# Optimization experiments

Measured on AMD Instinct MI355X. Metric: run time of the kernel, lower is better.

Reference implementation:

```python
import jax, jax.numpy as jnp
import numpy as np

HEAD_SIZE = 64
INPUT_SIZE = 1024
B, T = 8, 2048


def setup_inputs() -> dict:
    key = jax.random.key(0)
    kx, kq, kk, kv = jax.random.split(key, 4)
    x = jax.random.normal(kx, (B, T, INPUT_SIZE), dtype=jnp.float32)
    s = 1.0 / np.sqrt(INPUT_SIZE)
    Wq = jax.random.uniform(kq, (INPUT_SIZE, HEAD_SIZE), minval=-s, maxval=s, dtype=jnp.float32)
    Wk = jax.random.uniform(kk, (INPUT_SIZE, HEAD_SIZE), minval=-s, maxval=s, dtype=jnp.float32)
    Wv = jax.random.uniform(kv, (INPUT_SIZE, HEAD_SIZE), minval=-s, maxval=s, dtype=jnp.float32)
    return {"x": x, "Wq": Wq, "Wk": Wk, "Wv": Wv}


def reference(x, Wq, Wk, Wv):
    # Faithful to the torch module: scores = K @ Q^T (note: keys times queries^T),
    # causal mask on upper triangle of that matrix, softmax over last axis,
    # dropout treated as identity (eval), then scores @ V.
    q = jnp.einsum('bti,ih->bth', x, Wq)  # [B,T,H]
    k = jnp.einsum('bti,ih->bth', x, Wk)
    v = jnp.einsum('bti,ih->bth', x, Wv)
    scale = HEAD_SIZE ** -0.5
    scores = jnp.einsum('bth,bsh->bts', k, q) * scale  # [B,T,T] = K Q^T
    Tlen = x.shape[1]
    causal = jnp.tril(jnp.ones((Tlen, Tlen), dtype=bool))
    scores = jnp.where(causal, scores, -jnp.inf)
    w = jax.nn.softmax(scores, axis=-1)
    out = jnp.einsum('bts,bsh->bth', w, v)  # [B,T,H]
    return out
```

## Files before the change

kernel.cpp:

```cpp
#include <hip/hip_runtime.h>

typedef __bf16 bf16_t;
typedef bf16_t bf16x8 __attribute__((ext_vector_type(8)));
typedef float f32x4 __attribute__((ext_vector_type(4)));

#define NB 8
#define TT 2048
#define DIN 1024
#define HH 64
#define MM (NB * TT)

__device__ __forceinline__ unsigned short f2bf(float f) {
    unsigned int u = __float_as_uint(f);
    u += 0x7fffu + ((u >> 16) & 1u);
    return (unsigned short)(u >> 16);
}

__device__ __forceinline__ void async16(void* l, const void* g) {
    __builtin_amdgcn_global_load_lds(
        (const __attribute__((address_space(1))) unsigned int*)g,
        (__attribute__((address_space(3))) unsigned int*)l, 16, 0, 0);
}

__device__ __forceinline__ int block_detect_f32(const unsigned int* __restrict__ xw,
                                                int tid, int* sflag) {
    if (tid < 64) {
        unsigned int u = xw[tid];
        unsigned int e = (u >> 7) & 0xFFu;
        unsigned long long m = __ballot(e >= 100u && e <= 150u);
        if (tid == 0) *sflag = (__popcll(m) < 48) ? 1 : 0;
    }
    __syncthreads();
    return *sflag;
}

__global__ __launch_bounds__(256) void transpose_w_kernel(
    const void* __restrict__ Wq, const void* __restrict__ Wk,
    const void* __restrict__ Wv, const unsigned int* __restrict__ xw,
    unsigned short* __restrict__ Wt) {
    __shared__ int sflag;
    __shared__ unsigned short ts[64][68];
    const int tid = threadIdx.x;
    const int isf32 = block_detect_f32(xw, tid, &sflag);
    const int w = blockIdx.x >> 4, kt = blockIdx.x & 15;
    const void* W = (w == 0) ? Wq : (w == 1) ? Wk : Wv;
    const int kk = tid >> 4, nn = (tid & 15) * 4;
#pragma unroll
    for (int j = 0; j < 4; ++j) {
        int k = kk + j * 16;
        if (isf32) {
            float4 f = *(const float4*)((const float*)W + (size_t)(kt * 64 + k) * 64 + nn);
            ts[k][nn + 0] = f2bf(f.x); ts[k][nn + 1] = f2bf(f.y);
            ts[k][nn + 2] = f2bf(f.z); ts[k][nn + 3] = f2bf(f.w);
        } else {
            *(uint2*)&ts[k][nn] =
                *(const uint2*)((const unsigned short*)W + (size_t)(kt * 64 + k) * 64 + nn);
        }
    }
    __syncthreads();
    const int n = tid >> 2, k0 = (tid & 3) * 16;
    unsigned short tmp[16];
#pragma unroll
    for (int j = 0; j < 16; ++j) tmp[j] = ts[k0 + j][n];
    unsigned short* dst = Wt + (size_t)(w * 64 + n) * 1024 + kt * 64 + k0;
    *(uint4*)(dst + 0) = *(uint4*)&tmp[0];
    *(uint4*)(dst + 8) = *(uint4*)&tmp[8];
}

#define XR 72
#define WROWC 9

__global__ __launch_bounds__(256, 4) void proj_kernel(
    const void* __restrict__ xraw, const unsigned short* __restrict__ Wt,
    unsigned short* __restrict__ qbuf, unsigned short* __restrict__ kbuf,
    unsigned short* __restrict__ vtbuf) {
    __shared__ int sflag;
    __shared__ __align__(16) unsigned short xs[64 * XR];
    __shared__ __align__(16) unsigned char wlds[96 * WROWC * 16];

    const int tid = threadIdx.x;
    const int isf32 = block_detect_f32((const unsigned int*)xraw, tid, &sflag);
    const int m0 = blockIdx.x * 64;
    const int nh = blockIdx.y;
    const int wave = tid >> 6, lane = tid & 63, quad = lane >> 4, l15 = lane & 15;
    const int rw = wave & 1, cw = wave >> 1;

    const float* xf = (const float*)xraw;
    const unsigned short* xb = (const unsigned short*)xraw;
    const unsigned char* wg = (const unsigned char*)Wt;

    const unsigned char* wsrc[4];
    unsigned int wdst[4];
    int nw = 0;
#pragma unroll
    for (int j = 0; j < 4; ++j) {
        int c = (wave + 4 * j) * 64 + lane;
        if (c < 864) {
            int R = c / WROWC, cc = c % WROWC;
            int ccu = (cc > 7) ? 0 : cc;
            wsrc[nw] = wg + (size_t)(nh * 96 + R) * 2048 + ccu * 16;
            wdst[nw] = c * 16;
            ++nw;
        }
    }

    const int xr = tid >> 2, xc = (tid & 3) * 16;

    auto ldx = [&](int k0, float4 (&px)[4], uint4 (&pxb)[2]) {
        if (isf32) {
            const float* g = xf + (size_t)(m0 + xr) * DIN + k0 + xc;
#pragma unroll
            for (int j = 0; j < 4; ++j) px[j] = *(const float4*)(g + j * 4);
        } else {
            const unsigned short* g = xb + (size_t)(m0 + xr) * DIN + k0 + xc;
            pxb[0] = *(const uint4*)(g + 0);
            pxb[1] = *(const uint4*)(g + 8);
        }
    };
    auto writeX = [&](float4 (&px)[4], uint4 (&pxb)[2]) {
        if (isf32) {
            unsigned short t[16];
#pragma unroll
            for (int j = 0; j < 4; ++j) {
                t[j * 4 + 0] = f2bf(px[j].x); t[j * 4 + 1] = f2bf(px[j].y);
                t[j * 4 + 2] = f2bf(px[j].z); t[j * 4 + 3] = f2bf(px[j].w);
            }
            *(uint4*)&xs[xr * XR + xc + 0] = *(uint4*)&t[0];
            *(uint4*)&xs[xr * XR + xc + 8] = *(uint4*)&t[8];
        } else {
            *(uint4*)&xs[xr * XR + xc + 0] = pxb[0];
            *(uint4*)&xs[xr * XR + xc + 8] = pxb[1];
        }
    };

    f32x4 acc[2][3];
#pragma unroll
    for (int rt = 0; rt < 2; ++rt)
#pragma unroll
        for (int ct = 0; ct < 3; ++ct)
            acc[rt][ct] = (f32x4){0.f, 0.f, 0.f, 0.f};

    auto compute = [&]() {
#pragma unroll
        for (int ks = 0; ks < 2; ++ks) {
            bf16x8 a[2], b[3];
#pragma unroll
            for (int rt = 0; rt < 2; ++rt)
                a[rt] = *(const bf16x8*)
                    &xs[(rw * 32 + rt * 16 + l15) * XR + ks * 32 + quad * 8];
#pragma unroll
            for (int ct = 0; ct < 3; ++ct)
                b[ct] = *(const bf16x8*)
                    &wlds[(cw * 48 + ct * 16 + l15) * (WROWC * 16) + ks * 64 + quad * 16];
#pragma unroll
            for (int rt = 0; rt < 2; ++rt)
#pragma unroll
                for (int ct = 0; ct < 3; ++ct)
                    acc[rt][ct] = __builtin_amdgcn_mfma_f32_16x16x32_bf16(
                        a[rt], b[ct], acc[rt][ct], 0, 0, 0);
        }
    };

    auto step = [&](int it, float4 (&px)[4], uint4 (&pxb)[2]) {
        __syncthreads();
        writeX(px, pxb);
        const size_t off = (size_t)it * 128;
        for (int j = 0; j < nw; ++j) async16(&wlds[wdst[j]], wsrc[j] + off);
        __syncthreads();
        if (it < 14) ldx((it + 2) * 64, px, pxb);
        compute();
    };

    float4 pxA[4], pxB[4];
    uint4  pbA[2], pbB[2];
    ldx(0, pxA, pbA);
    ldx(64, pxB, pbB);

    for (int itp = 0; itp < 16; itp += 2) {
        step(itp + 0, pxA, pbA);
        step(itp + 1, pxB, pbB);
    }

#pragma unroll
    for (int rt = 0; rt < 2; ++rt)
#pragma unroll
        for (int ct = 0; ct < 3; ++ct) {
            int n = nh * 96 + cw * 48 + ct * 16 + l15;
            int wsel = n >> 6, nn = n & 63;
#pragma unroll
            for (int reg = 0; reg < 4; ++reg) {
                int m = m0 + rw * 32 + rt * 16 + quad * 4 + reg;
                unsigned short bv = f2bf(acc[rt][ct][reg]);
                if (wsel == 0)      qbuf[(size_t)m * HH + nn] = bv;
                else if (wsel == 1) kbuf[(size_t)m * HH + nn] = bv;
                else {
                    int bb = m >> 11, t = m & 2047;
                    vtbuf[((size_t)bb * HH + nn) * TT + t] = bv;
                }
            }
        }
}

__global__ __launch_bounds__(256, 4) void attn_kernel(
    const unsigned short* __restrict__ rowbuf,
    const unsigned short* __restrict__ colbuf,
    const unsigned short* __restrict__ vtbuf,
    float* __restrict__ O_part,
    float* __restrict__ l_part) {

    __shared__ __align__(16) unsigned short Qr_s[64][72];
    __shared__ __align__(16) unsigned short Kc_s[64][72];
    __shared__ __align__(16) unsigned short Vt_s[64][72];
    __shared__ __align__(16) unsigned short P_s[4][16][72];

    const int tid  = threadIdx.x;
    const int bid  = blockIdx.x;
    const int b    = bid & 7;
    const int bx   = bid >> 3;
    int rt, ch;
    if (bx < 8)       { rt = bx;                 ch = 0; }
    else if (bx < 24) { rt = 8 + ((bx - 8) >> 1);  ch = (bx - 8) & 1; }
    else if (bx < 48) { rt = 16 + (bx - 24) / 3;   ch = (bx - 24) % 3; }
    else              { rt = 24 + ((bx - 48) >> 2); ch = (bx - 48) & 3; }
    const int nct = min(8, rt + 1 - ch * 8);
    const int t0 = rt * 64;
    const int slot = b * 80 + bx;

    const int wave = tid >> 6, lane = tid & 63, quad = lane >> 4, l15 = lane & 15;
    const int sr = tid >> 2, sc = (tid & 3) * 16;

    {
        const uint4* g = (const uint4*)(rowbuf + ((size_t)b * TT + t0 + sr) * HH + sc);
        *(uint4*)&Qr_s[sr][sc + 0] = g[0];
        *(uint4*)&Qr_s[sr][sc + 8] = g[1];
    }

    f32x4 o[4];
#pragma unroll
    for (int c = 0; c < 4; ++c) o[c] = (f32x4){0.f, 0.f, 0.f, 0.f};
    float ls[4] = {0.f, 0.f, 0.f, 0.f};

    const float SCL2 = 0.125f * 1.4426950408889634f;

    uint4 pk0, pk1, pv0, pv1;
    auto loadKV = [&](int i) {
        const int s0 = (ch * 8 + i) * 64;
        const uint4* gk = (const uint4*)(colbuf + ((size_t)b * TT + s0 + sr) * HH + sc);
        pk0 = gk[0]; pk1 = gk[1];
        const uint4* gv = (const uint4*)(vtbuf + ((size_t)b * HH + sr) * TT + s0 + sc);
        pv0 = gv[0]; pv1 = gv[1];
    };
    loadKV(0);

    for (int i = 0; i < nct; ++i) {
        const int stc = ch * 8 + i;
        const int s0 = stc * 64;
        *(uint4*)&Kc_s[sr][sc + 0] = pk0;
        *(uint4*)&Kc_s[sr][sc + 8] = pk1;
        *(uint4*)&Vt_s[sr][sc + 0] = pv0;
        *(uint4*)&Vt_s[sr][sc + 8] = pv1;
        __syncthreads();

        f32x4 scf[4];
#pragma unroll
        for (int c = 0; c < 4; ++c) scf[c] = (f32x4){0.f, 0.f, 0.f, 0.f};
        __builtin_amdgcn_s_setprio(1);
#pragma unroll
        for (int ks = 0; ks < 2; ++ks) {
            bf16x8 a = *(const bf16x8*)&Qr_s[wave * 16 + l15][ks * 32 + quad * 8];
#pragma unroll
            for (int c = 0; c < 4; ++c) {
                bf16x8 bb = *(const bf16x8*)&Kc_s[c * 16 + l15][ks * 32 + quad * 8];
                scf[c] = __builtin_amdgcn_mfma_f32_16x16x32_bf16(a, bb, scf[c], 0, 0, 0);
            }
        }
        __builtin_amdgcn_s_setprio(0);

        if (i + 1 < nct) loadKV(i + 1);

        const bool diag = (stc == rt);
#pragma unroll
        for (int r = 0; r < 4; ++r) {
            const int tg = t0 + wave * 16 + quad * 4 + r;
#pragma unroll
            for (int c = 0; c < 4; ++c) {
                float arg = fmaf(scf[c][r], SCL2, -30.f);
                if (diag && (s0 + c * 16 + l15) > tg) arg = -200.f;
                float p = __builtin_amdgcn_exp2f(arg);
                P_s[wave][quad * 4 + r][c * 16 + l15] = f2bf(p);
                ls[r] += p;
            }
        }
        __builtin_amdgcn_s_setprio(1);
#pragma unroll
        for (int ks = 0; ks < 2; ++ks) {
            bf16x8 ap = *(const bf16x8*)&P_s[wave][l15][ks * 32 + quad * 8];
#pragma unroll
            for (int c = 0; c < 4; ++c) {
                bf16x8 bv = *(const bf16x8*)&Vt_s[c * 16 + l15][ks * 32 + quad * 8];
                o[c] = __builtin_amdgcn_mfma_f32_16x16x32_bf16(ap, bv, o[c], 0, 0, 0);
            }
        }
        __builtin_amdgcn_s_setprio(0);
        __syncthreads();
    }

#pragma unroll
    for (int r = 0; r < 4; ++r) {
#pragma unroll
        for (int off = 1; off < 16; off <<= 1) ls[r] += __shfl_xor(ls[r], off);
    }
    if (l15 == 0) {
#pragma unroll
        for (int r = 0; r < 4; ++r)
            l_part[(size_t)slot * 64 + wave * 16 + quad * 4 + r] = ls[r];
    }
#pragma unroll
    for (int c = 0; c < 4; ++c)
#pragma unroll
        for (int r = 0; r < 4; ++r)
            O_part[(size_t)slot * 4096 + (wave * 16 + quad * 4 + r) * 64 + c * 16 + l15] = o[c][r];
}

__global__ __launch_bounds__(256) void combine_kernel(
    const float* __restrict__ O_part, const float* __restrict__ l_part,
    const unsigned int* __restrict__ xw, void* __restrict__ outraw) {
    __shared__ int sflag;
    const int tid = threadIdx.x;
    const int isf32 = block_detect_f32(xw, tid, &sflag);
    const int bid = blockIdx.x;
    const int b = bid & 7, rt = bid >> 3;
    const int nch = rt / 8 + 1;
    const int off = (rt < 8) ? rt : (rt < 16) ? 8 + 2 * (rt - 8)
                   : (rt < 24) ? 24 + 3 * (rt - 16) : 48 + 4 * (rt - 24);
    const int slot0 = b * 80 + off;

    const int row = tid >> 2, cb = (tid & 3) * 16;
    f32x4 a[4];
#pragma unroll
    for (int q = 0; q < 4; ++q) a[q] = (f32x4){0.f, 0.f, 0.f, 0.f};
    float l = 0.f;
    for (int j = 0; j < nch; ++j) {
        const f32x4* p = (const f32x4*)(O_part + (size_t)(slot0 + j) * 4096 + row * 64 + cb);
#pragma unroll
        for (int q = 0; q < 4; ++q) a[q] += p[q];
        l += l_part[(size_t)(slot0 + j) * 64 + row];
    }
    const float inv = 1.f / l;
    const size_t base = ((size_t)b * TT + rt * 64 + row) * HH + cb;
    if (isf32) {
        float* outf = (float*)outraw;
#pragma unroll
        for (int q = 0; q < 4; ++q) {
            f32x4 v = a[q] * inv;
            *(f32x4*)(outf + base + q * 4) = v;
        }
    } else {
        unsigned short h[16];
#pragma unroll
        for (int q = 0; q < 4; ++q)
#pragma unroll
            for (int e = 0; e < 4; ++e) h[q * 4 + e] = f2bf(a[q][e] * inv);
        unsigned short* outb = (unsigned short*)outraw;
        *(uint4*)(outb + base + 0) = *(uint4*)&h[0];
        *(uint4*)(outb + base + 8) = *(uint4*)&h[8];
    }
}

extern "C" void kernel_launch(void* const* d_in, const int* in_sizes, int n_in,
                              void* d_out, int out_size, void* d_ws, size_t ws_size,
                              hipStream_t stream) {
    const void* x  = d_in[0];
    const void* Wq = d_in[1];
    const void* Wk = d_in[2];
    const void* Wv = d_in[3];
    unsigned short* ws = (unsigned short*)d_ws;

    unsigned short* qbuf  = ws;
    unsigned short* kbuf  = ws + (size_t)MM * HH;
    unsigned short* vtbuf = ws + (size_t)2 * MM * HH;
    unsigned short* wtbuf = ws + (size_t)3 * MM * HH;
    float* O_part = (float*)(ws + (size_t)3 * MM * HH + 3 * 65536);
    float* l_part = O_part + (size_t)640 * 4096;

    hipLaunchKernelGGL(transpose_w_kernel, dim3(48), dim3(256), 0, stream,
                       Wq, Wk, Wv, (const unsigned int*)x, wtbuf);
    hipLaunchKernelGGL(proj_kernel, dim3(256, 2), dim3(256), 0, stream,
                       x, wtbuf, qbuf, kbuf, vtbuf);
    hipLaunchKernelGGL(attn_kernel, dim3(640), dim3(256), 0, stream,
                       kbuf, qbuf, vtbuf, O_part, l_part);
    hipLaunchKernelGGL(combine_kernel, dim3(256), dim3(256), 0, stream,
                       O_part, l_part, (const unsigned int*)x, d_out);
}
```

Measured before the change: 154.5 us.

## Shrink projection N-tile to 48 columns and drop double-buffered x prefetch

The projection kernel now splits the 192 output columns into four 48-wide tiles instead of two 96-wide tiles, so it launches twice as many blocks. Each wave now computes a 16x48 slice instead of 32x48. The x prefetch goes from a two-deep register double buffer to a single stage, and launch bounds drop to 2 blocks per CU. The goal is more parallelism and less register pressure, at the cost of reading x twice as many times from global memory and having less latency hiding per block.

```diff
diff --git a/kernel.cpp b/kernel.cpp
--- a/kernel.cpp
+++ b/kernel.cpp
@@ -69,44 +69,45 @@
 
 #define XR 72
 #define WROWC 9
-
-__global__ __launch_bounds__(256, 4) void proj_kernel(
+#define PN 48
+
+__global__ __launch_bounds__(256, 2) void proj_kernel(
     const void* __restrict__ xraw, const unsigned short* __restrict__ Wt,
     unsigned short* __restrict__ qbuf, unsigned short* __restrict__ kbuf,
     unsigned short* __restrict__ vtbuf) {
     __shared__ int sflag;
     __shared__ __align__(16) unsigned short xs[64 * XR];
-    __shared__ __align__(16) unsigned char wlds[96 * WROWC * 16];
+    __shared__ __align__(16) unsigned char wlds[PN * WROWC * 16];
 
     const int tid = threadIdx.x;
     const int isf32 = block_detect_f32((const unsigned int*)xraw, tid, &sflag);
     const int m0 = blockIdx.x * 64;
     const int nh = blockIdx.y;
     const int wave = tid >> 6, lane = tid & 63, quad = lane >> 4, l15 = lane & 15;
-    const int rw = wave & 1, cw = wave >> 1;
 
     const float* xf = (const float*)xraw;
     const unsigned short* xb = (const unsigned short*)xraw;
     const unsigned char* wg = (const unsigned char*)Wt;
 
-    const unsigned char* wsrc[4];
-    unsigned int wdst[4];
+    const unsigned char* wsrc[2];
+    unsigned int wdst[2];
     int nw = 0;
 #pragma unroll
-    for (int j = 0; j < 4; ++j) {
+    for (int j = 0; j < 2; ++j) {
         int c = (wave + 4 * j) * 64 + lane;
-        if (c < 864) {
+        if (c < PN * WROWC) {
             int R = c / WROWC, cc = c % WROWC;
             int ccu = (cc > 7) ? 0 : cc;
-            wsrc[nw] = wg + (size_t)(nh * 96 + R) * 2048 + ccu * 16;
+            wsrc[nw] = wg + (size_t)(nh * PN + R) * 2048 + ccu * 16;
             wdst[nw] = c * 16;
             ++nw;
         }
     }
 
     const int xr = tid >> 2, xc = (tid & 3) * 16;
-
-    auto ldx = [&](int k0, float4 (&px)[4], uint4 (&pxb)[2]) {
+    float4 px[4];
+    uint4  pxb[2];
+    auto ldx = [&](int k0) {
         if (isf32) {
             const float* g = xf + (size_t)(m0 + xr) * DIN + k0 + xc;
 #pragma unroll
@@ -117,7 +118,15 @@
             pxb[1] = *(const uint4*)(g + 8);
         }
     };
-    auto writeX = [&](float4 (&px)[4], uint4 (&pxb)[2]) {
+
+    f32x4 acc[3];
+#pragma unroll
+    for (int ct = 0; ct < 3; ++ct) acc[ct] = (f32x4){0.f, 0.f, 0.f, 0.f};
+
+    ldx(0);
+    size_t woff = 0;
+    for (int it = 0; it < 16; ++it) {
+        __syncthreads();
         if (isf32) {
             unsigned short t[16];
 #pragma unroll
@@ -131,74 +140,43 @@
             *(uint4*)&xs[xr * XR + xc + 0] = pxb[0];
             *(uint4*)&xs[xr * XR + xc + 8] = pxb[1];
         }
-    };
-
-    f32x4 acc[2][3];
-#pragma unroll
-    for (int rt = 0; rt < 2; ++rt)
-#pragma unroll
-        for (int ct = 0; ct < 3; ++ct)
-            acc[rt][ct] = (f32x4){0.f, 0.f, 0.f, 0.f};
-
-    auto compute = [&]() {
+        for (int j = 0; j < nw; ++j) async16(&wlds[wdst[j]], wsrc[j] + woff);
+        woff += 128;
+        __syncthreads();
+
+        if (it < 15) ldx((it + 1) * 64);
+
 #pragma unroll
         for (int ks = 0; ks < 2; ++ks) {
-            bf16x8 a[2], b[3];
-#pragma unroll
-            for (int rt = 0; rt < 2; ++rt)
-                a[rt] = *(const bf16x8*)
-                    &xs[(rw * 32 + rt * 16 + l15) * XR + ks * 32 + quad * 8];
+            bf16x8 a = *(const bf16x8*)&xs[(wave * 16 + l15) * XR + ks * 32 + quad * 8];
+            bf16x8 b[3];
 #pragma unroll
             for (int ct = 0; ct < 3; ++ct)
                 b[ct] = *(const bf16x8*)
-                    &wlds[(cw * 48 + ct * 16 + l15) * (WROWC * 16) + ks * 64 + quad * 16];
-#pragma unroll
-            for (int rt = 0; rt < 2; ++rt)
-#pragma unroll
-                for (int ct = 0; ct < 3; ++ct)
-                    acc[rt][ct] = __builtin_amdgcn_mfma_f32_16x16x32_bf16(
-                        a[rt], b[ct], acc[rt][ct], 0, 0, 0);
-        }
-    };
-
-    auto step = [&](int it, float4 (&px)[4], uint4 (&pxb)[2]) {
-        __syncthreads();
-        writeX(px, pxb);
-        const size_t off = (size_t)it * 128;
-        for (int j = 0; j < nw; ++j) async16(&wlds[wdst[j]], wsrc[j] + off);
-        __syncthreads();
-        if (it < 14) ldx((it + 2) * 64, px, pxb);
-        compute();
-    };
-
-    float4 pxA[4], pxB[4];
-    uint4  pbA[2], pbB[2];
-    ldx(0, pxA, pbA);
-    ldx(64, pxB, pbB);
-
-    for (int itp = 0; itp < 16; itp += 2) {
-        step(itp + 0, pxA, pbA);
-        step(itp + 1, pxB, pbB);
-    }
-
-#pragma unroll
-    for (int rt = 0; rt < 2; ++rt)
-#pragma unroll
-        for (int ct = 0; ct < 3; ++ct) {
-            int n = nh * 96 + cw * 48 + ct * 16 + l15;
-            int wsel = n >> 6, nn = n & 63;
-#pragma unroll
-            for (int reg = 0; reg < 4; ++reg) {
-                int m = m0 + rw * 32 + rt * 16 + quad * 4 + reg;
-                unsigned short bv = f2bf(acc[rt][ct][reg]);
-                if (wsel == 0)      qbuf[(size_t)m * HH + nn] = bv;
-                else if (wsel == 1) kbuf[(size_t)m * HH + nn] = bv;
-                else {
-                    int bb = m >> 11, t = m & 2047;
-                    vtbuf[((size_t)bb * HH + nn) * TT + t] = bv;
-                }
-            }
-        }
+                    &wlds[(ct * 16 + l15) * (WROWC * 16) + ks * 64 + quad * 16];
+#pragma unroll
+            for (int ct = 0; ct < 3; ++ct)
+                acc[ct] = __builtin_amdgcn_mfma_f32_16x16x32_bf16(
+                    a, b[ct], acc[ct], 0, 0, 0);
+        }
+    }
+
+#pragma unroll
+    for (int ct = 0; ct < 3; ++ct) {
+        int n = nh * PN + ct * 16 + l15;
+        int wsel = n >> 6, nn = n & 63;
+#pragma unroll
+        for (int reg = 0; reg < 4; ++reg) {
+            int m = m0 + wave * 16 + quad * 4 + reg;
+            unsigned short bv = f2bf(acc[ct][reg]);
+            if (wsel == 0)      qbuf[(size_t)m * HH + nn] = bv;
+            else if (wsel == 1) kbuf[(size_t)m * HH + nn] = bv;
+            else {
+                int bb = m >> 11, t = m & 2047;
+                vtbuf[((size_t)bb * HH + nn) * TT + t] = bv;
+            }
+        }
+    }
 }
 
 __global__ __launch_bounds__(256, 4) void attn_kernel(
@@ -385,7 +363,7 @@
 
     hipLaunchKernelGGL(transpose_w_kernel, dim3(48), dim3(256), 0, stream,
                        Wq, Wk, Wv, (const unsigned int*)x, wtbuf);
-    hipLaunchKernelGGL(proj_kernel, dim3(256, 2), dim3(256), 0, stream,
+    hipLaunchKernelGGL(proj_kernel, dim3(256, 4), dim3(256), 0, stream,
                        x, wtbuf, qbuf, kbuf, vtbuf);
     hipLaunchKernelGGL(attn_kernel, dim3(640), dim3(256), 0, stream,
                        kbuf, qbuf, vtbuf, O_part, l_part);
```

After: 144.7 us. 1.07x faster.
